# Optimization experiments

Measured on AMD Instinct MI355X. Metric: run time of the kernel, lower is better.

## Reference

```python
import jax, jax.numpy as jnp
import numpy as np

N_NODES = 100000


def setup_inputs() -> dict:
    key = jax.random.key(0)
    ks = jax.random.split(key, 6)
    F_IN, F_CH, F_OUT = 64, 64, 64
    E = 1200000
    x = jax.random.normal(ks[0], (N_NODES, F_IN), dtype=jnp.float32)
    edge_index = jax.random.randint(ks[1], (2, E), 0, N_NODES, dtype=jnp.int64)
    # MLP params (PyTorch Linear default init scale ~ 1/sqrt(fan_in))
    s1 = 1.0 / np.sqrt(2 * F_IN)
    s2 = 1.0 / np.sqrt(F_CH)
    W1 = jax.random.uniform(ks[2], (2 * F_IN, F_CH), jnp.float32, -s1, s1)
    b1 = jax.random.uniform(ks[3], (F_CH,), jnp.float32, -s1, s1)
    W2 = jax.random.uniform(ks[4], (F_CH, F_OUT), jnp.float32, -s2, s2)
    b2 = jax.random.uniform(ks[5], (F_OUT,), jnp.float32, -s2, s2)
    return {"x": x, "edge_index": edge_index, "W1": W1, "b1": b1, "W2": W2, "b2": b2}


def reference(x, edge_index, W1, b1, W2, b2):
    # PyG EdgeConv with aggr='add': out_i = sum_j MLP(concat[x_i, x_j - x_i])
    src = edge_index[0]  # j (source / neighbor)
    dst = edge_index[1]  # i (target, aggregation index)
    x_i = x[dst]                     # [E, F]
    x_j = x[src]                     # [E, F]
    msg = jnp.concatenate([x_i, x_j - x_i], axis=-1)      # [E, 2F]
    h = jax.nn.relu(msg @ W1 + b1) @ W2 + b2               # [E, F_out]
    agg = jax.ops.segment_sum(h, dst, num_segments=N_NODES)  # [N, F_out]
    return jnp.tanh(agg)
```

## Files before the change

### kernel.cpp

```cpp
#include <hip/hip_runtime.h>
#include <math.h>


#define FDIM 64
#define BN 64
#define BSH 6
#define CAPB 1024
#define MAXB 2048
#define EPB 4096
#define PRE_SMEM 24576

typedef unsigned int u32;
typedef unsigned short u16;
typedef _Float16 hf;
typedef _Float16 h2 __attribute__((ext_vector_type(2)));

__device__ __forceinline__ float bf_lo(u32 u) {
    union { u32 i; float f; } c; c.i = u << 16; return c.f;
}
__device__ __forceinline__ float bf_hi(u32 u) {
    union { u32 i; float f; } c; c.i = u & 0xffff0000u; return c.f;
}
__device__ __forceinline__ u32 f2bf_rne(float f) {
    union { float f; u32 u; } c; c.f = f;
    u32 u = c.u;
    u += 0x7fffu + ((u >> 16) & 1u);
    return u >> 16;
}
__device__ __forceinline__ u32 f2h(float f) {
    union { u16 s; hf h; } c; c.h = (hf)f; return (u32)c.s;
}
__device__ __forceinline__ float h_lo(u32 u) {
    union { u16 s; hf h; } c; c.s = (u16)(u & 0xffffu); return (float)c.h;
}
__device__ __forceinline__ float h_hi(u32 u) {
    union { u16 s; hf h; } c; c.s = (u16)(u >> 16); return (float)c.h;
}
__device__ __forceinline__ h2 u2h2(u32 u) {
    union { u32 u; h2 h; } c; c.u = u; return c.h;
}

__global__ __launch_bounds__(256) void wprep_k(
    const float* __restrict__ W1, const float* __restrict__ W2,
    u32* __restrict__ Wchg, u32* __restrict__ W2hg)
{
    const int tid = threadIdx.x;
    for (int i = tid; i < 4096; i += 256) {
        int kk = i >> 7, c = i & 127;
        int k0 = 2 * kk, k1 = 2 * kk + 1;
        float a0, a1;
        if (c < 64) {
            a0 = W1[k0 * 64 + c] - W1[(64 + k0) * 64 + c];
            a1 = W1[k1 * 64 + c] - W1[(64 + k1) * 64 + c];
        } else {
            int cc = c - 64;
            a0 = W1[(64 + k0) * 64 + cc];
            a1 = W1[(64 + k1) * 64 + cc];
        }
        Wchg[i] = f2h(a0) | (f2h(a1) << 16);
    }
    for (int i = tid; i < 2048; i += 256) {
        int k = i >> 5, c2 = i & 31;
        W2hg[i] = f2h(W2[k * 64 + c2 * 2]) | (f2h(W2[k * 64 + c2 * 2 + 1]) << 16);
    }
}

__global__ __launch_bounds__(256) void prep_k(
    const float* __restrict__ x, const u32* __restrict__ Wchg,
    const float* __restrict__ b1, u16* __restrict__ Ah,
    u16* __restrict__ Bmh, const int* __restrict__ ei,
    u32* __restrict__ slotB, int* __restrict__ gcnt,
    int N, int E, int NB, int nPre, int nBin)
{
    __shared__ __align__(16) char smem[PRE_SMEM];
    const int idx = blockIdx.x;
    const int tid = threadIdx.x;

    if ((idx % 6) == 5) {
        const int bb = idx / 6;
        if (bb >= nBin) return;
        int* histL = (int*)smem;
        int* gbase = histL + MAXB;
        const int e0 = bb * EPB;

        for (int j = tid; j < NB; j += 256) histL[j] = 0;
        __syncthreads();

        #pragma unroll 8
        for (int i = 0; i < EPB / 256; ++i) {
            int e = e0 + i * 256 + tid;
            if (e < E) {
                int d = ei[E + e];
                atomicAdd(&histL[d >> BSH], 1);
            }
        }
        __syncthreads();

        for (int j = tid; j < NB; j += 256) {
            int h = histL[j];
            gbase[j] = (h > 0) ? atomicAdd(&gcnt[j], h) : 0;
            histL[j] = 0;
        }
        __syncthreads();

        #pragma unroll 8
        for (int i = 0; i < EPB / 256; ++i) {
            int e = e0 + i * 256 + tid;
            if (e < E) {
                int s = ei[e];
                int d = ei[E + e];
                int b = d >> BSH;
                int pos = gbase[b] + atomicAdd(&histL[b], 1);
                if (pos < CAPB)
                    slotB[(size_t)b * CAPB + pos] =
                        ((u32)(d & (BN - 1)) << 20) | (u32)s;
            }
        }
        return;
    }

    const int pb = idx - idx / 6;
    if (pb >= nPre) return;
    u32 (*Wch)[128] = (u32(*)[128])smem;
    u32* xs = (u32*)(smem + 16384);

    const int node0 = pb * 64;

    {
        const uint4* Wg4 = (const uint4*)Wchg;
        #pragma unroll
        for (int it = 0; it < 4; ++it) {
            int i = it * 256 + tid;
            uint4 w = Wg4[i];
            *(uint4*)&Wch[i >> 5][(i & 31) * 4] = w;
        }
    }
    {
        const float4* X4 = (const float4*)x;
        #pragma unroll
        for (int it = 0; it < 4; ++it) {
            int i = it * 256 + tid;
            int n = i >> 4, k4 = i & 15;
            int gn = node0 + n;
            float4 v = make_float4(0.f, 0.f, 0.f, 0.f);
            if (gn < N) v = X4[(size_t)gn * 16 + k4];
            int r0 = 2 * k4, r1 = 2 * k4 + 1;
            int g = n >> 2, lo = n & 3;
            xs[r0 * 64 + (((g ^ (r0 & 15)) << 2) | lo)] = f2h(v.x) | (f2h(v.y) << 16);
            xs[r1 * 64 + (((g ^ (r1 & 15)) << 2) | lo)] = f2h(v.z) | (f2h(v.w) << 16);
        }
    }
    __syncthreads();

    const int ng = tid & 15, cg = tid >> 4;
    const int n0 = ng * 4, c0 = cg * 8;

    float acc[4][8];
    #pragma unroll
    for (int ci = 0; ci < 8; ++ci) {
        float init = (c0 < 64) ? b1[c0 + ci] : 0.f;
        #pragma unroll
        for (int ni = 0; ni < 4; ++ni) acc[ni][ci] = init;
    }

    #pragma unroll 4
    for (int kk = 0; kk < 32; ++kk) {
        uint4 xq = *(const uint4*)&xs[kk * 64 + ((ng ^ (kk & 15)) << 2)];
        uint4 w0 = *(const uint4*)&Wch[kk][c0];
        uint4 w1 = *(const uint4*)&Wch[kk][c0 + 4];
        h2 wv[8] = {u2h2(w0.x), u2h2(w0.y), u2h2(w0.z), u2h2(w0.w),
                    u2h2(w1.x), u2h2(w1.y), u2h2(w1.z), u2h2(w1.w)};
        u32 xv[4] = {xq.x, xq.y, xq.z, xq.w};
        #pragma unroll
        for (int ni = 0; ni < 4; ++ni) {
            h2 xh = u2h2(xv[ni]);
            #pragma unroll
            for (int ci = 0; ci < 8; ++ci)
                acc[ni][ci] = __builtin_amdgcn_fdot2(xh, wv[ci], acc[ni][ci], false);
        }
    }

    #pragma unroll
    for (int ni = 0; ni < 4; ++ni) {
        int n = node0 + n0 + ni;
        if (n >= N) break;
        if (c0 < 64) {
            uint4 pk;
            pk.x = f2h(acc[ni][0]) | (f2h(acc[ni][1]) << 16);
            pk.y = f2h(acc[ni][2]) | (f2h(acc[ni][3]) << 16);
            pk.z = f2h(acc[ni][4]) | (f2h(acc[ni][5]) << 16);
            pk.w = f2h(acc[ni][6]) | (f2h(acc[ni][7]) << 16);
            *(uint4*)&Ah[(size_t)n * 64 + c0] = pk;
        } else {
            uint4 pk;
            pk.x = f2bf_rne(acc[ni][0]) | (f2bf_rne(acc[ni][1]) << 16);
            pk.y = f2bf_rne(acc[ni][2]) | (f2bf_rne(acc[ni][3]) << 16);
            pk.z = f2bf_rne(acc[ni][4]) | (f2bf_rne(acc[ni][5]) << 16);
            pk.w = f2bf_rne(acc[ni][6]) | (f2bf_rne(acc[ni][7]) << 16);
            *(uint4*)&Bmh[(size_t)n * 64 + (c0 - 64)] = pk;
        }
    }
}

__device__ __forceinline__ float4 relu4add(float4 acc, float4 a, float4 b) {
    acc.x += fmaxf(a.x + b.x, 0.f);
    acc.y += fmaxf(a.y + b.y, 0.f);
    acc.z += fmaxf(a.z + b.z, 0.f);
    acc.w += fmaxf(a.w + b.w, 0.f);
    return acc;
}
__device__ __forceinline__ float4 relu4add_m(float4 acc, float4 a, float4 b, bool m) {
    acc.x += m ? fmaxf(a.x + b.x, 0.f) : 0.f;
    acc.y += m ? fmaxf(a.y + b.y, 0.f) : 0.f;
    acc.z += m ? fmaxf(a.z + b.z, 0.f) : 0.f;
    acc.w += m ? fmaxf(a.w + b.w, 0.f) : 0.f;
    return acc;
}
__device__ __forceinline__ float4 bf4(uint2 u) {
    return make_float4(bf_lo(u.x), bf_hi(u.x), bf_lo(u.y), bf_hi(u.y));
}

__global__ __launch_bounds__(256) void fused_agg(
    const u16* __restrict__ Ah, const u16* __restrict__ Bmh,
    const u32* __restrict__ slotB, const int* __restrict__ gcnt,
    const u32* __restrict__ W2hg, const float* __restrict__ b2,
    float* __restrict__ out, int N)
{
    __shared__ __align__(16) u32 W2h[64][34];
    __shared__ __align__(16) u32 pool[BN * 17 * 2];
    __shared__ u32 csrS[CAPB];
    __shared__ int histL[BN];
    __shared__ int rowO[BN + 1];
    __shared__ int ofs[BN];
    __shared__ float b2s[64];

    u32* eStage = pool;
    uint2* aggTb = (uint2*)pool;

    const int tid = threadIdx.x;
    const int b = blockIdx.x;
    const int node0 = b * BN;
    const int cntB = min(gcnt[b], CAPB);

    {
        const uint4* Wg4 = (const uint4*)W2hg;
        #pragma unroll
        for (int it = 0; it < 2; ++it) {
            int i = it * 256 + tid;
            uint4 w = Wg4[i];
            *(uint4*)&W2h[i >> 3][(i & 7) * 4] = w;
        }
    }
    if (tid < 64) b2s[tid] = b2[tid];
    if (tid < BN) histL[tid] = 0;
    __syncthreads();

    for (int i = tid; i < cntB; i += 256) {
        u32 e = slotB[(size_t)b * CAPB + i];
        eStage[i] = e;
        atomicAdd(&histL[e >> 20], 1);
    }
    __syncthreads();

    if (tid < 32) {
        int l = tid;
        int h0 = histL[2 * l], h1 = histL[2 * l + 1];
        int s = h0 + h1, inc = s;
        #pragma unroll
        for (int off = 1; off < 32; off <<= 1) {
            int t = __shfl_up(inc, off);
            if (l >= off) inc += t;
        }
        int base = inc - s;
        rowO[2 * l] = base; rowO[2 * l + 1] = base + h0;
        ofs[2 * l] = base;  ofs[2 * l + 1] = base + h0;
        if (l == 31) rowO[BN] = inc;
    }
    __syncthreads();

    for (int i = tid; i < cntB; i += 256) {
        u32 e = eStage[i];
        int pos = atomicAdd(&ofs[e >> 20], 1);
        csrS[pos] = e & 0xFFFFFu;
    }
    __syncthreads();

    {
        const int q = tid & 15, ng = tid >> 4;
        const uint2* __restrict__ B2 = (const uint2*)Bmh;
        const uint2* __restrict__ A2 = (const uint2*)Ah;
        #pragma unroll
        for (int h = 0; h < 4; ++h) {
            int nl = ng + h * 16;
            int gn = node0 + nl;
            int start = rowO[nl];
            int d = (gn < N) ? (rowO[nl + 1] - start) : 0;
            float4 a = make_float4(0.f, 0.f, 0.f, 0.f);
            if (gn < N) {
                uint2 ua = A2[(size_t)gn * 16 + q];
                a = make_float4(h_lo(ua.x), h_hi(ua.x), h_lo(ua.y), h_hi(ua.y));
            }
            float4 acc = make_float4(0.f, 0.f, 0.f, 0.f);

            int j = 0;
            for (; j + 8 <= d; j += 8) {
                int ss[8];
                uint2 bb[8];
                #pragma unroll
                for (int t = 0; t < 8; ++t) ss[t] = csrS[start + j + t];
                #pragma unroll
                for (int t = 0; t < 8; ++t) bb[t] = B2[(size_t)ss[t] * 16 + q];
                #pragma unroll
                for (int t = 0; t < 8; ++t) acc = relu4add(acc, a, bf4(bb[t]));
            }
            if (j < d) {
                int ss[8];
                uint2 bb[8];
                #pragma unroll
                for (int t = 0; t < 8; ++t) ss[t] = csrS[start + min(j + t, d - 1)];
                #pragma unroll
                for (int t = 0; t < 8; ++t) bb[t] = B2[(size_t)ss[t] * 16 + q];
                acc = relu4add(acc, a, bf4(bb[0]));
                #pragma unroll
                for (int t = 1; t < 8; ++t)
                    acc = relu4add_m(acc, a, bf4(bb[t]), j + t < d);
            }
            uint2 pk;
            pk.x = f2h(acc.x) | (f2h(acc.y) << 16);
            pk.y = f2h(acc.z) | (f2h(acc.w) << 16);
            aggTb[nl * 17 + q] = pk;
        }
    }
    __syncthreads();

    {
        const int cg = tid & 15, g = tid >> 4;
        const int c0 = cg * 4;
        const int nb0 = g * 4;
        float o[4][4];
        #pragma unroll
        for (int ni = 0; ni < 4; ++ni) {
            float dg = (float)(rowO[nb0 + ni + 1] - rowO[nb0 + ni]);
            #pragma unroll
            for (int ci = 0; ci < 4; ++ci) o[ni][ci] = dg * b2s[c0 + ci];
        }
        #pragma unroll 2
        for (int kc = 0; kc < 16; ++kc) {
            uint2 u0 = aggTb[(nb0 + 0) * 17 + kc];
            uint2 u1 = aggTb[(nb0 + 1) * 17 + kc];
            uint2 u2 = aggTb[(nb0 + 2) * 17 + kc];
            uint2 u3 = aggTb[(nb0 + 3) * 17 + kc];
            #pragma unroll
            for (int kk = 0; kk < 4; ++kk) {
                uint2 w2p = *(const uint2*)&W2h[kc * 4 + kk][cg * 2];
                float wv[4] = {h_lo(w2p.x), h_hi(w2p.x), h_lo(w2p.y), h_hi(w2p.y)};
                float a0 = (kk < 2) ? ((kk == 0) ? h_lo(u0.x) : h_hi(u0.x))
                                    : ((kk == 2) ? h_lo(u0.y) : h_hi(u0.y));
                float a1 = (kk < 2) ? ((kk == 0) ? h_lo(u1.x) : h_hi(u1.x))
                                    : ((kk == 2) ? h_lo(u1.y) : h_hi(u1.y));
                float a2 = (kk < 2) ? ((kk == 0) ? h_lo(u2.x) : h_hi(u2.x))
                                    : ((kk == 2) ? h_lo(u2.y) : h_hi(u2.y));
                float a3 = (kk < 2) ? ((kk == 0) ? h_lo(u3.x) : h_hi(u3.x))
                                    : ((kk == 2) ? h_lo(u3.y) : h_hi(u3.y));
                #pragma unroll
                for (int ci = 0; ci < 4; ++ci) {
                    o[0][ci] += a0 * wv[ci];
                    o[1][ci] += a1 * wv[ci];
                    o[2][ci] += a2 * wv[ci];
                    o[3][ci] += a3 * wv[ci];
                }
            }
        }
        #pragma unroll
        for (int ni = 0; ni < 4; ++ni) {
            int gn = node0 + nb0 + ni;
            if (gn < N) {
                float4 r = make_float4(tanhf(o[ni][0]), tanhf(o[ni][1]),
                                       tanhf(o[ni][2]), tanhf(o[ni][3]));
                ((float4*)out)[(size_t)gn * 16 + cg] = r;
            }
        }
    }
}

extern "C" void kernel_launch(void* const* d_in, const int* in_sizes, int n_in,
                              void* d_out, int out_size, void* d_ws, size_t ws_size,
                              hipStream_t stream)
{
    const float* x  = (const float*)d_in[0];
    const int*   ei = (const int*)d_in[1];
    const float* W1 = (const float*)d_in[2];
    const float* b1 = (const float*)d_in[3];
    const float* W2 = (const float*)d_in[4];
    const float* b2 = (const float*)d_in[5];
    float* out = (float*)d_out;

    const int N = in_sizes[0] / FDIM;
    const int E = in_sizes[1] / 2;
    const int NB = (N + BN - 1) / BN;

    u16*   Ah    = (u16*)d_ws;
    u16*   Bmh   = Ah + (size_t)N * FDIM;
    u32*   slotB = (u32*)(Bmh + (size_t)N * FDIM);
    u32*   Wchg  = slotB + (size_t)NB * CAPB;
    u32*   W2hg  = Wchg + 4096;
    int*   gcnt  = (int*)(W2hg + 2048);

    hipMemsetAsync(gcnt, 0, (size_t)NB * sizeof(int), stream);

    wprep_k<<<1, 256, 0, stream>>>(W1, W2, Wchg, W2hg);

    const int nPre = (N + 63) / 64;
    const int nBin = (E + EPB - 1) / EPB;
    int T = (nPre * 6 + 4) / 5;
    while (T - T / 6 < nPre) ++T;
    if (T < 6 * nBin) T = 6 * nBin;

    prep_k<<<T, 256, 0, stream>>>(x, Wchg, b1, Ah, Bmh, ei, slotB, gcnt,
                                  N, E, NB, nPre, nBin);
    fused_agg<<<NB, 256, 0, stream>>>(Ah, Bmh, slotB, gcnt, W2hg, b2, out, N);
}
```

Before: 179.5 us.

## Fold weight prep into prep and aggregation kernels, process two node tiles per block

Removes the single-block weight-prep kernel launch: prep blocks now build the combined fp16 W1 matrix directly in shared memory, and each aggregation block converts W2 itself. Each node-transform block now handles two 64-node tiles, prefetching the second tile's x into registers while the first is computed, which amortises the per-block W1 conversion. The block interleave changes from 5:1 to 3:1 node-to-binning blocks. The cost is redundant W1/W2 fp32-to-fp16 conversion in every block, plus more shared memory per prep block.

```diff
diff --git a/kernel.cpp b/kernel.cpp
--- a/kernel.cpp
+++ b/kernel.cpp
@@ -8,7 +8,9 @@
 #define CAPB 1024
 #define MAXB 2048
 #define EPB 4096
-#define PRE_SMEM 24576
+#define NT 64
+#define TPB 2
+#define PRE_SMEM 32768
 
 typedef unsigned int u32;
 typedef unsigned short u16;
@@ -40,33 +42,8 @@
     union { u32 u; h2 h; } c; c.u = u; return c.h;
 }
 
-__global__ __launch_bounds__(256) void wprep_k(
-    const float* __restrict__ W1, const float* __restrict__ W2,
-    u32* __restrict__ Wchg, u32* __restrict__ W2hg)
-{
-    const int tid = threadIdx.x;
-    for (int i = tid; i < 4096; i += 256) {
-        int kk = i >> 7, c = i & 127;
-        int k0 = 2 * kk, k1 = 2 * kk + 1;
-        float a0, a1;
-        if (c < 64) {
-            a0 = W1[k0 * 64 + c] - W1[(64 + k0) * 64 + c];
-            a1 = W1[k1 * 64 + c] - W1[(64 + k1) * 64 + c];
-        } else {
-            int cc = c - 64;
-            a0 = W1[(64 + k0) * 64 + cc];
-            a1 = W1[(64 + k1) * 64 + cc];
-        }
-        Wchg[i] = f2h(a0) | (f2h(a1) << 16);
-    }
-    for (int i = tid; i < 2048; i += 256) {
-        int k = i >> 5, c2 = i & 31;
-        W2hg[i] = f2h(W2[k * 64 + c2 * 2]) | (f2h(W2[k * 64 + c2 * 2 + 1]) << 16);
-    }
-}
-
 __global__ __launch_bounds__(256) void prep_k(
-    const float* __restrict__ x, const u32* __restrict__ Wchg,
+    const float* __restrict__ x, const float* __restrict__ W1,
     const float* __restrict__ b1, u16* __restrict__ Ah,
     u16* __restrict__ Bmh, const int* __restrict__ ei,
     u32* __restrict__ slotB, int* __restrict__ gcnt,
@@ -76,8 +53,8 @@
     const int idx = blockIdx.x;
     const int tid = threadIdx.x;
 
-    if ((idx % 6) == 5) {
-        const int bb = idx / 6;
+    if ((idx & 3) == 3) {
+        const int bb = idx >> 2;
         if (bb >= nBin) return;
         int* histL = (int*)smem;
         int* gbase = histL + MAXB;
@@ -119,87 +96,123 @@
         return;
     }
 
-    const int pb = idx - idx / 6;
+    const int pb = idx - (idx >> 2);
     if (pb >= nPre) return;
     u32 (*Wch)[128] = (u32(*)[128])smem;
     u32* xs = (u32*)(smem + 16384);
 
-    const int node0 = pb * 64;
-
-    {
-        const uint4* Wg4 = (const uint4*)Wchg;
-        #pragma unroll
-        for (int it = 0; it < 4; ++it) {
-            int i = it * 256 + tid;
-            uint4 w = Wg4[i];
-            *(uint4*)&Wch[i >> 5][(i & 31) * 4] = w;
-        }
-    }
-    {
-        const float4* X4 = (const float4*)x;
-        #pragma unroll
-        for (int it = 0; it < 4; ++it) {
-            int i = it * 256 + tid;
-            int n = i >> 4, k4 = i & 15;
-            int gn = node0 + n;
-            float4 v = make_float4(0.f, 0.f, 0.f, 0.f);
-            if (gn < N) v = X4[(size_t)gn * 16 + k4];
-            int r0 = 2 * k4, r1 = 2 * k4 + 1;
-            int g = n >> 2, lo = n & 3;
-            xs[r0 * 64 + (((g ^ (r0 & 15)) << 2) | lo)] = f2h(v.x) | (f2h(v.y) << 16);
-            xs[r1 * 64 + (((g ^ (r1 & 15)) << 2) | lo)] = f2h(v.z) | (f2h(v.w) << 16);
-        }
-    }
-    __syncthreads();
+    const int node0 = pb * (NT * TPB);
+    const float4* X4 = (const float4*)x;
+
+    float4 xv[4];
+    #pragma unroll
+    for (int it = 0; it < 4; ++it) {
+        int i = it * 256 + tid;
+        int n = i >> 4, k4 = i & 15;
+        int gn = node0 + n;
+        xv[it] = (gn < N) ? X4[(size_t)gn * 16 + k4]
+                          : make_float4(0.f, 0.f, 0.f, 0.f);
+    }
+
+    for (int i = tid; i < 4096; i += 256) {
+        int kk = i >> 7, c = i & 127;
+        int k0 = 2 * kk, k1 = k0 + 1;
+        float a0, a1;
+        if (c < 64) {
+            a0 = W1[k0 * 64 + c] - W1[(64 + k0) * 64 + c];
+            a1 = W1[k1 * 64 + c] - W1[(64 + k1) * 64 + c];
+        } else {
+            int cc = c - 64;
+            a0 = W1[(64 + k0) * 64 + cc];
+            a1 = W1[(64 + k1) * 64 + cc];
+        }
+        Wch[kk][c] = f2h(a0) | (f2h(a1) << 16);
+    }
+
+    #pragma unroll
+    for (int it = 0; it < 4; ++it) {
+        int i = it * 256 + tid;
+        int n = i >> 4, k4 = i & 15;
+        int r0 = 2 * k4, r1 = r0 + 1;
+        int g = n >> 2, lo = n & 3;
+        xs[r0 * 64 + (((g ^ (r0 & 15)) << 2) | lo)] = f2h(xv[it].x) | (f2h(xv[it].y) << 16);
+        xs[r1 * 64 + (((g ^ (r1 & 15)) << 2) | lo)] = f2h(xv[it].z) | (f2h(xv[it].w) << 16);
+    }
+    __syncthreads();
+
+    #pragma unroll
+    for (int it = 0; it < 4; ++it) {
+        int i = it * 256 + tid;
+        int n = i >> 4, k4 = i & 15;
+        int gn = node0 + NT + n;
+        xv[it] = (gn < N) ? X4[(size_t)gn * 16 + k4]
+                          : make_float4(0.f, 0.f, 0.f, 0.f);
+    }
 
     const int ng = tid & 15, cg = tid >> 4;
     const int n0 = ng * 4, c0 = cg * 8;
 
-    float acc[4][8];
+    auto compute_store = [&](const u32* xst, int base) {
+        float acc[4][8];
+        #pragma unroll
+        for (int ci = 0; ci < 8; ++ci) {
+            float init = (c0 < 64) ? b1[c0 + ci] : 0.f;
+            #pragma unroll
+            for (int ni = 0; ni < 4; ++ni) acc[ni][ci] = init;
+        }
+        #pragma unroll 4
+        for (int kk = 0; kk < 32; ++kk) {
+            uint4 xq = *(const uint4*)&xst[kk * 64 + ((ng ^ (kk & 15)) << 2)];
+            uint4 w0 = *(const uint4*)&Wch[kk][c0];
+            uint4 w1 = *(const uint4*)&Wch[kk][c0 + 4];
+            h2 wv[8] = {u2h2(w0.x), u2h2(w0.y), u2h2(w0.z), u2h2(w0.w),
+                        u2h2(w1.x), u2h2(w1.y), u2h2(w1.z), u2h2(w1.w)};
+            u32 xq4[4] = {xq.x, xq.y, xq.z, xq.w};
+            #pragma unroll
+            for (int ni = 0; ni < 4; ++ni) {
+                h2 xh = u2h2(xq4[ni]);
+                #pragma unroll
+                for (int ci = 0; ci < 8; ++ci)
+                    acc[ni][ci] = __builtin_amdgcn_fdot2(xh, wv[ci], acc[ni][ci], false);
+            }
+        }
+        #pragma unroll
+        for (int ni = 0; ni < 4; ++ni) {
+            int n = base + n0 + ni;
+            if (n >= N) break;
+            if (c0 < 64) {
+                uint4 pk;
+                pk.x = f2h(acc[ni][0]) | (f2h(acc[ni][1]) << 16);
+                pk.y = f2h(acc[ni][2]) | (f2h(acc[ni][3]) << 16);
+                pk.z = f2h(acc[ni][4]) | (f2h(acc[ni][5]) << 16);
+                pk.w = f2h(acc[ni][6]) | (f2h(acc[ni][7]) << 16);
+                *(uint4*)&Ah[(size_t)n * 64 + c0] = pk;
+            } else {
+                uint4 pk;
+                pk.x = f2bf_rne(acc[ni][0]) | (f2bf_rne(acc[ni][1]) << 16);
+                pk.y = f2bf_rne(acc[ni][2]) | (f2bf_rne(acc[ni][3]) << 16);
+                pk.z = f2bf_rne(acc[ni][4]) | (f2bf_rne(acc[ni][5]) << 16);
+                pk.w = f2bf_rne(acc[ni][6]) | (f2bf_rne(acc[ni][7]) << 16);
+                *(uint4*)&Bmh[(size_t)n * 64 + (c0 - 64)] = pk;
+            }
+        }
+    };
+
+    compute_store(xs, node0);
+
+    u32* xs1 = xs + 2048;
     #pragma unroll
-    for (int ci = 0; ci < 8; ++ci) {
-        float init = (c0 < 64) ? b1[c0 + ci] : 0.f;
-        #pragma unroll
-        for (int ni = 0; ni < 4; ++ni) acc[ni][ci] = init;
-    }
-
-    #pragma unroll 4
-    for (int kk = 0; kk < 32; ++kk) {
-        uint4 xq = *(const uint4*)&xs[kk * 64 + ((ng ^ (kk & 15)) << 2)];
-        uint4 w0 = *(const uint4*)&Wch[kk][c0];
-        uint4 w1 = *(const uint4*)&Wch[kk][c0 + 4];
-        h2 wv[8] = {u2h2(w0.x), u2h2(w0.y), u2h2(w0.z), u2h2(w0.w),
-                    u2h2(w1.x), u2h2(w1.y), u2h2(w1.z), u2h2(w1.w)};
-        u32 xv[4] = {xq.x, xq.y, xq.z, xq.w};
-        #pragma unroll
-        for (int ni = 0; ni < 4; ++ni) {
-            h2 xh = u2h2(xv[ni]);
-            #pragma unroll
-            for (int ci = 0; ci < 8; ++ci)
-                acc[ni][ci] = __builtin_amdgcn_fdot2(xh, wv[ci], acc[ni][ci], false);
-        }
-    }
-
-    #pragma unroll
-    for (int ni = 0; ni < 4; ++ni) {
-        int n = node0 + n0 + ni;
-        if (n >= N) break;
-        if (c0 < 64) {
-            uint4 pk;
-            pk.x = f2h(acc[ni][0]) | (f2h(acc[ni][1]) << 16);
-            pk.y = f2h(acc[ni][2]) | (f2h(acc[ni][3]) << 16);
-            pk.z = f2h(acc[ni][4]) | (f2h(acc[ni][5]) << 16);
-            pk.w = f2h(acc[ni][6]) | (f2h(acc[ni][7]) << 16);
-            *(uint4*)&Ah[(size_t)n * 64 + c0] = pk;
-        } else {
-            uint4 pk;
-            pk.x = f2bf_rne(acc[ni][0]) | (f2bf_rne(acc[ni][1]) << 16);
-            pk.y = f2bf_rne(acc[ni][2]) | (f2bf_rne(acc[ni][3]) << 16);
-            pk.z = f2bf_rne(acc[ni][4]) | (f2bf_rne(acc[ni][5]) << 16);
-            pk.w = f2bf_rne(acc[ni][6]) | (f2bf_rne(acc[ni][7]) << 16);
-            *(uint4*)&Bmh[(size_t)n * 64 + (c0 - 64)] = pk;
-        }
-    }
+    for (int it = 0; it < 4; ++it) {
+        int i = it * 256 + tid;
+        int n = i >> 4, k4 = i & 15;
+        int r0 = 2 * k4, r1 = r0 + 1;
+        int g = n >> 2, lo = n & 3;
+        xs1[r0 * 64 + (((g ^ (r0 & 15)) << 2) | lo)] = f2h(xv[it].x) | (f2h(xv[it].y) << 16);
+        xs1[r1 * 64 + (((g ^ (r1 & 15)) << 2) | lo)] = f2h(xv[it].z) | (f2h(xv[it].w) << 16);
+    }
+    __syncthreads();
+
+    compute_store(xs1, node0 + NT);
 }
 
 __device__ __forceinline__ float4 relu4add(float4 acc, float4 a, float4 b) {
@@ -223,7 +236,7 @@
 __global__ __launch_bounds__(256) void fused_agg(
     const u16* __restrict__ Ah, const u16* __restrict__ Bmh,
     const u32* __restrict__ slotB, const int* __restrict__ gcnt,
-    const u32* __restrict__ W2hg, const float* __restrict__ b2,
+    const float* __restrict__ W2, const float* __restrict__ b2,
     float* __restrict__ out, int N)
 {
     __shared__ __align__(16) u32 W2h[64][34];
@@ -242,14 +255,9 @@
     const int node0 = b * BN;
     const int cntB = min(gcnt[b], CAPB);
 
-    {
-        const uint4* Wg4 = (const uint4*)W2hg;
-        #pragma unroll
-        for (int it = 0; it < 2; ++it) {
-            int i = it * 256 + tid;
-            uint4 w = Wg4[i];
-            *(uint4*)&W2h[i >> 3][(i & 7) * 4] = w;
-        }
+    for (int i = tid; i < 2048; i += 256) {
+        int k = i >> 5, c2 = i & 31;
+        W2h[k][c2] = f2h(W2[k * 64 + 2 * c2]) | (f2h(W2[k * 64 + 2 * c2 + 1]) << 16);
     }
     if (tid < 64) b2s[tid] = b2[tid];
     if (tid < BN) histL[tid] = 0;
@@ -402,21 +410,16 @@
     u16*   Ah    = (u16*)d_ws;
     u16*   Bmh   = Ah + (size_t)N * FDIM;
     u32*   slotB = (u32*)(Bmh + (size_t)N * FDIM);
-    u32*   Wchg  = slotB + (size_t)NB * CAPB;
-    u32*   W2hg  = Wchg + 4096;
-    int*   gcnt  = (int*)(W2hg + 2048);
+    int*   gcnt  = (int*)(slotB + (size_t)NB * CAPB);
 
     hipMemsetAsync(gcnt, 0, (size_t)NB * sizeof(int), stream);
 
-    wprep_k<<<1, 256, 0, stream>>>(W1, W2, Wchg, W2hg);
-
-    const int nPre = (N + 63) / 64;
+    const int nPre = (N + NT * TPB - 1) / (NT * TPB);
     const int nBin = (E + EPB - 1) / EPB;
-    int T = (nPre * 6 + 4) / 5;
-    while (T - T / 6 < nPre) ++T;
-    if (T < 6 * nBin) T = 6 * nBin;
-
-    prep_k<<<T, 256, 0, stream>>>(x, Wchg, b1, Ah, Bmh, ei, slotB, gcnt,
+    int T = 4 * nBin;
+    while (T - T / 4 < nPre) ++T;
+
+    prep_k<<<T, 256, 0, stream>>>(x, W1, b1, Ah, Bmh, ei, slotB, gcnt,
                                   N, E, NB, nPre, nBin);
-    fused_agg<<<NB, 256, 0, stream>>>(Ah, Bmh, slotB, gcnt, W2hg, b2, out, N);
-}
+    fused_agg<<<NB, 256, 0, stream>>>(Ah, Bmh, slotB, gcnt, W2, b2, out, N);
+}
```

Result: slower. 193.1 us (+7.6%).

## Compute per-node A-projection inside aggregation kernel and drop weight-prep kernel

Applied to the files above, without the earlier changes.

The A = x·(W1a−W1b)+b1 projection moves out of the prep kernel into the fused aggregation kernel. Each aggregation block now recomputes it for its own 64 nodes from x and W1, so the fp16 A buffer is neither written to nor read from global memory. The separate weight-prep launch is removed: weights are converted to half precision inside each kernel, and prep_k now produces only the B projection. The cost is extra matmul work and weight conversion per aggregation block, plus shared-memory aliasing between the staged weights/x and the CSR staging buffers.

```diff
diff --git a/kernel.cpp b/kernel.cpp
--- a/kernel.cpp
+++ b/kernel.cpp
@@ -8,7 +8,7 @@
 #define CAPB 1024
 #define MAXB 2048
 #define EPB 4096
-#define PRE_SMEM 24576
+#define PRE_SMEM 16384
 
 typedef unsigned int u32;
 typedef unsigned short u16;
@@ -40,34 +40,8 @@
     union { u32 u; h2 h; } c; c.u = u; return c.h;
 }
 
-__global__ __launch_bounds__(256) void wprep_k(
-    const float* __restrict__ W1, const float* __restrict__ W2,
-    u32* __restrict__ Wchg, u32* __restrict__ W2hg)
-{
-    const int tid = threadIdx.x;
-    for (int i = tid; i < 4096; i += 256) {
-        int kk = i >> 7, c = i & 127;
-        int k0 = 2 * kk, k1 = 2 * kk + 1;
-        float a0, a1;
-        if (c < 64) {
-            a0 = W1[k0 * 64 + c] - W1[(64 + k0) * 64 + c];
-            a1 = W1[k1 * 64 + c] - W1[(64 + k1) * 64 + c];
-        } else {
-            int cc = c - 64;
-            a0 = W1[(64 + k0) * 64 + cc];
-            a1 = W1[(64 + k1) * 64 + cc];
-        }
-        Wchg[i] = f2h(a0) | (f2h(a1) << 16);
-    }
-    for (int i = tid; i < 2048; i += 256) {
-        int k = i >> 5, c2 = i & 31;
-        W2hg[i] = f2h(W2[k * 64 + c2 * 2]) | (f2h(W2[k * 64 + c2 * 2 + 1]) << 16);
-    }
-}
-
 __global__ __launch_bounds__(256) void prep_k(
-    const float* __restrict__ x, const u32* __restrict__ Wchg,
-    const float* __restrict__ b1, u16* __restrict__ Ah,
+    const float* __restrict__ x, const float* __restrict__ W1,
     u16* __restrict__ Bmh, const int* __restrict__ ei,
     u32* __restrict__ slotB, int* __restrict__ gcnt,
     int N, int E, int NB, int nPre, int nBin)
@@ -121,19 +95,16 @@
 
     const int pb = idx - idx / 6;
     if (pb >= nPre) return;
-    u32 (*Wch)[128] = (u32(*)[128])smem;
-    u32* xs = (u32*)(smem + 16384);
+    u32 (*Wch)[64] = (u32(*)[64])smem;
+    u32* xs = (u32*)(smem + 8192);
 
     const int node0 = pb * 64;
 
-    {
-        const uint4* Wg4 = (const uint4*)Wchg;
-        #pragma unroll
-        for (int it = 0; it < 4; ++it) {
-            int i = it * 256 + tid;
-            uint4 w = Wg4[i];
-            *(uint4*)&Wch[i >> 5][(i & 31) * 4] = w;
-        }
+    for (int i = tid; i < 2048; i += 256) {
+        int kk = i >> 6, c = i & 63;
+        float a0 = W1[(64 + 2 * kk) * 64 + c];
+        float a1 = W1[(64 + 2 * kk + 1) * 64 + c];
+        ((u32*)smem)[i] = f2h(a0) | (f2h(a1) << 16);
     }
     {
         const float4* X4 = (const float4*)x;
@@ -144,7 +115,7 @@
             int gn = node0 + n;
             float4 v = make_float4(0.f, 0.f, 0.f, 0.f);
             if (gn < N) v = X4[(size_t)gn * 16 + k4];
-            int r0 = 2 * k4, r1 = 2 * k4 + 1;
+            int r0 = 2 * k4, r1 = r0 + 1;
             int g = n >> 2, lo = n & 3;
             xs[r0 * 64 + (((g ^ (r0 & 15)) << 2) | lo)] = f2h(v.x) | (f2h(v.y) << 16);
             xs[r1 * 64 + (((g ^ (r1 & 15)) << 2) | lo)] = f2h(v.z) | (f2h(v.w) << 16);
@@ -153,29 +124,25 @@
     __syncthreads();
 
     const int ng = tid & 15, cg = tid >> 4;
-    const int n0 = ng * 4, c0 = cg * 8;
-
-    float acc[4][8];
+    const int n0 = ng * 4, c0 = cg * 4;
+
+    float acc[4][4];
     #pragma unroll
-    for (int ci = 0; ci < 8; ++ci) {
-        float init = (c0 < 64) ? b1[c0 + ci] : 0.f;
-        #pragma unroll
-        for (int ni = 0; ni < 4; ++ni) acc[ni][ci] = init;
-    }
+    for (int ni = 0; ni < 4; ++ni)
+        #pragma unroll
+        for (int ci = 0; ci < 4; ++ci) acc[ni][ci] = 0.f;
 
     #pragma unroll 4
     for (int kk = 0; kk < 32; ++kk) {
         uint4 xq = *(const uint4*)&xs[kk * 64 + ((ng ^ (kk & 15)) << 2)];
-        uint4 w0 = *(const uint4*)&Wch[kk][c0];
-        uint4 w1 = *(const uint4*)&Wch[kk][c0 + 4];
-        h2 wv[8] = {u2h2(w0.x), u2h2(w0.y), u2h2(w0.z), u2h2(w0.w),
-                    u2h2(w1.x), u2h2(w1.y), u2h2(w1.z), u2h2(w1.w)};
-        u32 xv[4] = {xq.x, xq.y, xq.z, xq.w};
+        uint4 w = *(const uint4*)&Wch[kk][c0];
+        h2 wv[4] = {u2h2(w.x), u2h2(w.y), u2h2(w.z), u2h2(w.w)};
+        u32 xq4[4] = {xq.x, xq.y, xq.z, xq.w};
         #pragma unroll
         for (int ni = 0; ni < 4; ++ni) {
-            h2 xh = u2h2(xv[ni]);
+            h2 xh = u2h2(xq4[ni]);
             #pragma unroll
-            for (int ci = 0; ci < 8; ++ci)
+            for (int ci = 0; ci < 4; ++ci)
                 acc[ni][ci] = __builtin_amdgcn_fdot2(xh, wv[ci], acc[ni][ci], false);
         }
     }
@@ -184,21 +151,10 @@
     for (int ni = 0; ni < 4; ++ni) {
         int n = node0 + n0 + ni;
         if (n >= N) break;
-        if (c0 < 64) {
-            uint4 pk;
-            pk.x = f2h(acc[ni][0]) | (f2h(acc[ni][1]) << 16);
-            pk.y = f2h(acc[ni][2]) | (f2h(acc[ni][3]) << 16);
-            pk.z = f2h(acc[ni][4]) | (f2h(acc[ni][5]) << 16);
-            pk.w = f2h(acc[ni][6]) | (f2h(acc[ni][7]) << 16);
-            *(uint4*)&Ah[(size_t)n * 64 + c0] = pk;
-        } else {
-            uint4 pk;
-            pk.x = f2bf_rne(acc[ni][0]) | (f2bf_rne(acc[ni][1]) << 16);
-            pk.y = f2bf_rne(acc[ni][2]) | (f2bf_rne(acc[ni][3]) << 16);
-            pk.z = f2bf_rne(acc[ni][4]) | (f2bf_rne(acc[ni][5]) << 16);
-            pk.w = f2bf_rne(acc[ni][6]) | (f2bf_rne(acc[ni][7]) << 16);
-            *(uint4*)&Bmh[(size_t)n * 64 + (c0 - 64)] = pk;
-        }
+        uint2 pk;
+        pk.x = f2bf_rne(acc[ni][0]) | (f2bf_rne(acc[ni][1]) << 16);
+        pk.y = f2bf_rne(acc[ni][2]) | (f2bf_rne(acc[ni][3]) << 16);
+        *(uint2*)&Bmh[(size_t)n * 64 + c0] = pk;
     }
 }
 
@@ -221,38 +177,84 @@
 }
 
 __global__ __launch_bounds__(256) void fused_agg(
-    const u16* __restrict__ Ah, const u16* __restrict__ Bmh,
+    const float* __restrict__ x, const float* __restrict__ W1,
+    const float* __restrict__ b1, const u16* __restrict__ Bmh,
     const u32* __restrict__ slotB, const int* __restrict__ gcnt,
-    const u32* __restrict__ W2hg, const float* __restrict__ b2,
+    const float* __restrict__ W2, const float* __restrict__ b2,
     float* __restrict__ out, int N)
 {
+    __shared__ __align__(16) char uni[16384];
     __shared__ __align__(16) u32 W2h[64][34];
-    __shared__ __align__(16) u32 pool[BN * 17 * 2];
-    __shared__ u32 csrS[CAPB];
     __shared__ int histL[BN];
     __shared__ int rowO[BN + 1];
     __shared__ int ofs[BN];
     __shared__ float b2s[64];
-
-    u32* eStage = pool;
-    uint2* aggTb = (uint2*)pool;
+    __shared__ float b1s[64];
+
+    u32 (*Wdh)[64] = (u32(*)[64])uni;
+    u32* xs = (u32*)(uni + 8192);
+    u32* csrS = (u32*)uni;
+    u32* eStage = (u32*)(uni + 4096);
+    uint2* aggTb = (uint2*)(uni + 4096);
 
     const int tid = threadIdx.x;
     const int b = blockIdx.x;
     const int node0 = b * BN;
     const int cntB = min(gcnt[b], CAPB);
 
+    for (int i = tid; i < 2048; i += 256) {
+        int kk = i >> 6, c = i & 63;
+        int k0 = 2 * kk, k1 = k0 + 1;
+        float a0 = W1[k0 * 64 + c] - W1[(64 + k0) * 64 + c];
+        float a1 = W1[k1 * 64 + c] - W1[(64 + k1) * 64 + c];
+        ((u32*)uni)[i] = f2h(a0) | (f2h(a1) << 16);
+    }
     {
-        const uint4* Wg4 = (const uint4*)W2hg;
-        #pragma unroll
-        for (int it = 0; it < 2; ++it) {
+        const float4* X4 = (const float4*)x;
+        #pragma unroll
+        for (int it = 0; it < 4; ++it) {
             int i = it * 256 + tid;
-            uint4 w = Wg4[i];
-            *(uint4*)&W2h[i >> 3][(i & 7) * 4] = w;
-        }
-    }
-    if (tid < 64) b2s[tid] = b2[tid];
+            int n = i >> 4, k4 = i & 15;
+            int gn = node0 + n;
+            float4 v = make_float4(0.f, 0.f, 0.f, 0.f);
+            if (gn < N) v = X4[(size_t)gn * 16 + k4];
+            int r0 = 2 * k4, r1 = r0 + 1;
+            int g = n >> 2, lo = n & 3;
+            xs[r0 * 64 + (((g ^ (r0 & 15)) << 2) | lo)] = f2h(v.x) | (f2h(v.y) << 16);
+            xs[r1 * 64 + (((g ^ (r1 & 15)) << 2) | lo)] = f2h(v.z) | (f2h(v.w) << 16);
+        }
+    }
+    for (int i = tid; i < 2048; i += 256) {
+        int k = i >> 5, c2 = i & 31;
+        W2h[k][c2] = f2h(W2[k * 64 + 2 * c2]) | (f2h(W2[k * 64 + 2 * c2 + 1]) << 16);
+    }
+    if (tid < 64) { b2s[tid] = b2[tid]; b1s[tid] = b1[tid]; }
     if (tid < BN) histL[tid] = 0;
+    __syncthreads();
+
+    const int q = tid & 15, ng = tid >> 4;
+    const int q4 = q * 4;
+    float af[4][4];
+    #pragma unroll
+    for (int h = 0; h < 4; ++h)
+        #pragma unroll
+        for (int ci = 0; ci < 4; ++ci) af[h][ci] = b1s[q4 + ci];
+
+    #pragma unroll 4
+    for (int kk = 0; kk < 32; ++kk) {
+        uint4 wq = *(const uint4*)&Wdh[kk][q4];
+        h2 wv[4] = {u2h2(wq.x), u2h2(wq.y), u2h2(wq.z), u2h2(wq.w)};
+        #pragma unroll
+        for (int h = 0; h < 4; ++h) {
+            int n = ng + h * 16;
+            int g = n >> 2, lo = n & 3;
+            u32 xv = xs[kk * 64 + (((g ^ (kk & 15)) << 2) | lo)];
+            h2 xh = u2h2(xv);
+            #pragma unroll
+            for (int ci = 0; ci < 4; ++ci)
+                af[h][ci] = __builtin_amdgcn_fdot2(xh, wv[ci], af[h][ci], false);
+        }
+    }
     __syncthreads();
 
     for (int i = tid; i < cntB; i += 256) {
@@ -286,20 +288,14 @@
     __syncthreads();
 
     {
-        const int q = tid & 15, ng = tid >> 4;
         const uint2* __restrict__ B2 = (const uint2*)Bmh;
-        const uint2* __restrict__ A2 = (const uint2*)Ah;
         #pragma unroll
         for (int h = 0; h < 4; ++h) {
             int nl = ng + h * 16;
             int gn = node0 + nl;
             int start = rowO[nl];
             int d = (gn < N) ? (rowO[nl + 1] - start) : 0;
-            float4 a = make_float4(0.f, 0.f, 0.f, 0.f);
-            if (gn < N) {
-                uint2 ua = A2[(size_t)gn * 16 + q];
-                a = make_float4(h_lo(ua.x), h_hi(ua.x), h_lo(ua.y), h_hi(ua.y));
-            }
+            float4 a = make_float4(af[h][0], af[h][1], af[h][2], af[h][3]);
             float4 acc = make_float4(0.f, 0.f, 0.f, 0.f);
 
             int j = 0;
@@ -399,16 +395,11 @@
     const int E = in_sizes[1] / 2;
     const int NB = (N + BN - 1) / BN;
 
-    u16*   Ah    = (u16*)d_ws;
-    u16*   Bmh   = Ah + (size_t)N * FDIM;
+    u16*   Bmh   = (u16*)d_ws;
     u32*   slotB = (u32*)(Bmh + (size_t)N * FDIM);
-    u32*   Wchg  = slotB + (size_t)NB * CAPB;
-    u32*   W2hg  = Wchg + 4096;
-    int*   gcnt  = (int*)(W2hg + 2048);
+    int*   gcnt  = (int*)(slotB + (size_t)NB * CAPB);
 
     hipMemsetAsync(gcnt, 0, (size_t)NB * sizeof(int), stream);
-
-    wprep_k<<<1, 256, 0, stream>>>(W1, W2, Wchg, W2hg);
 
     const int nPre = (N + 63) / 64;
     const int nBin = (E + EPB - 1) / EPB;
@@ -416,7 +407,7 @@
     while (T - T / 6 < nPre) ++T;
     if (T < 6 * nBin) T = 6 * nBin;
 
-    prep_k<<<T, 256, 0, stream>>>(x, Wchg, b1, Ah, Bmh, ei, slotB, gcnt,
+    prep_k<<<T, 256, 0, stream>>>(x, W1, Bmh, ei, slotB, gcnt,
                                   N, E, NB, nPre, nBin);
-    fused_agg<<<NB, 256, 0, stream>>>(Ah, Bmh, slotB, gcnt, W2hg, b2, out, N);
-}
+    fused_agg<<<NB, 256, 0, stream>>>(x, W1, b1, Bmh, slotB, gcnt, W2, b2, out, N);
+}
```

Measured after the change: 185.6 us. 1.03x slower.
